# Kernel optimization log

Hardware: AMD Instinct MI355X
Metric: run time of the kernel (lower is better)

## Reference

```python
import jax, jax.numpy as jnp
import numpy as np

B, T, N, F = 4, 24, 1024, 96
H, HD = 3, 32      # spatial GATConv: 3 heads, head-dim 32 (averaged -> 32 per branch, 3 branches -> 96)
GH, GHD = 4, 24    # GroupedGAT: 4 heads concatenated -> 96
E = 8192           # edges per graph


def setup_inputs() -> dict:
    key = jax.random.key(0)
    ks = jax.random.split(key, 24)
    s_in = 1.0 / np.sqrt(F)
    def gat_params(k):
        k1, k2, k3, k4 = jax.random.split(k, 4)
        return (jax.random.normal(k1, (F, H * HD), jnp.float32) * s_in,
                jax.random.normal(k2, (H, HD), jnp.float32) * 0.1,
                jax.random.normal(k3, (H, HD), jnp.float32) * 0.1,
                jax.random.normal(k4, (H, HD), jnp.float32) * 0.02)
    W_d, al_d, ar_d, b_d = gat_params(ks[3])
    W_m, al_m, ar_m, b_m = gat_params(ks[4])
    W_s, al_s, ar_s, b_s = gat_params(ks[5])
    inp = {
        "input": jax.random.normal(ks[0], (B, T, N, F), jnp.float32),
        "spatial_embedding": jax.random.normal(ks[1], (B, T, N, F), jnp.float32),
        "temporal_embedding": jax.random.normal(ks[2], (B, T, N, F), jnp.float32),
        "src_d": jax.random.randint(ks[6], (E,), 0, N, jnp.int32),
        "dst_d": (jnp.arange(E) % N).astype(jnp.int32),
        "src_m": jax.random.randint(ks[7], (E,), 0, N, jnp.int32),
        "dst_m": (jnp.arange(E) % N).astype(jnp.int32),
        "src_s": jax.random.randint(ks[8], (E,), 0, N, jnp.int32),
        "dst_s": (jnp.arange(E) % N).astype(jnp.int32),
        "W_d": W_d, "al_d": al_d, "ar_d": ar_d, "b_d": b_d,
        "W_m": W_m, "al_m": al_m, "ar_m": ar_m, "b_m": b_m,
        "W_s": W_s, "al_s": al_s, "ar_s": ar_s, "b_s": b_s,
        "Wg": jax.random.normal(ks[9], (F, GH * GHD), jnp.float32) * s_in,
        "agl": jax.random.normal(ks[10], (GH, GHD), jnp.float32) * 0.1,
        "agr": jax.random.normal(ks[11], (GH, GHD), jnp.float32) * 0.1,
        "Wf": jax.random.normal(ks[12], (2 * F, F), jnp.float32) * (1.0 / np.sqrt(2 * F)),
        "bf": jnp.zeros((F,), jnp.float32),
    }
    return inp


def _gat(x, src, dst, W, al, ar, b):
    # x: (N, K, F) node features with K = T*B batched feature slots
    K = x.shape[1]
    h = (x @ W).reshape(N, K, H, HD)                       # (N,K,H,HD)
    el = (h * al).sum(-1)                                  # (N,K,H)
    er = (h * ar).sum(-1)
    e = jax.nn.leaky_relu(el[src] + er[dst], 0.2)          # (E,K,H)
    emax = jax.ops.segment_max(e, dst, num_segments=N)
    emax = jnp.where(jnp.isfinite(emax), emax, 0.0)
    ex = jnp.exp(e - emax[dst])
    denom = jax.ops.segment_sum(ex, dst, num_segments=N)
    alpha = ex / (denom[dst] + 1e-9)                       # edge softmax over incoming edges
    out = jax.ops.segment_sum(h[src] * alpha[..., None], dst, num_segments=N)
    return (out + b).mean(2)                               # average heads -> (N,K,HD)


def reference(input, spatial_embedding, temporal_embedding,
              src_d, dst_d, src_m, dst_m, src_s, dst_s,
              W_d, al_d, ar_d, b_d, W_m, al_m, ar_m, b_m, W_s, al_s, ar_s, b_s,
              Wg, agl, agr, Wf, bf):
    # ---------------- SpatialBlock ----------------
    residual_s = input                                     # input_dim == output_dim
    x_in = input + spatial_embedding
    # torch: input.transpose(0,2).reshape(N,-1,F) -> slot order is (t,b)
    x = jnp.transpose(x_in, (2, 1, 0, 3)).reshape(N, T * B, F)
    xd = _gat(x, src_d, dst_d, W_d, al_d, ar_d, b_d)
    xm = _gat(x, src_m, dst_m, W_m, al_m, ar_m, b_m)
    xs = _gat(x, src_s, dst_s, W_s, al_s, ar_s, b_s)
    x_attn = jnp.concatenate([xd, xm, xs], axis=-1)        # (N, T*B, 3*HD=F)
    # torch: transpose(0,1).reshape(batch,T,N,-1)  (keeps original (t,b) slot order quirk)
    x_attn = jnp.transpose(x_attn, (1, 0, 2)).reshape(B, T, N, F)
    cov0 = spatial_embedding[:, 0]                         # (B,N,F)
    attn_S = jax.nn.softmax(cov0 @ jnp.swapaxes(cov0, 1, 2), axis=2)  # (B,N,N)
    # NOTE: embedding_x branch in SpatialBlock is dead code (out is overwritten); skipped.
    spatial = residual_s + x_attn

    # ---------------- TemporalBlock ----------------
    residual_t = input
    xt = jnp.swapaxes(input, 1, 2).reshape(B * N, T, F)    # (B*N, T, F), index k=b*N+n
    # GroupedGAT: dense multi-head GAT over the T=period_num time steps
    hg = (xt @ Wg).reshape(B * N, T, GH, GHD)
    elg = (hg * agl).sum(-1)                               # (BN,T,GH)
    erg = (hg * agr).sum(-1)
    eg = jax.nn.leaky_relu(elg[:, :, None, :] + erg[:, None, :, :], 0.2)  # (BN,Ti,Tj,GH)
    alphag = jax.nn.softmax(eg, axis=2)
    xg = jnp.einsum('kijh,kjhd->kihd', alphag, hg).reshape(B * N, T, GH * GHD)
    covT = temporal_embedding[:, :, 0]                     # (B,T,F)
    attn_T = jax.nn.softmax(covT @ jnp.swapaxes(covT, 1, 2), axis=1)      # softmax over dim=1 as in torch
    # torch: attn.repeat(N,1,1) paired with x of batch index b*N+n -> uses attn[(b*N+n) % B]
    idx = (jnp.arange(B * N) % B)
    emb = jnp.einsum('kij,kjf->kif', attn_T[idx], xt)      # (BN,T,F)
    xg = xg * jax.nn.sigmoid(emb)
    xg = jnp.swapaxes(xg.reshape(B, N, T, F), 1, 2)        # (B,T,N,F)
    temporal = residual_t + xg

    # ---------------- Fusion ----------------
    z = jax.nn.sigmoid(jnp.concatenate([spatial, temporal], axis=-1) @ Wf + bf)
    out = z * spatial + (1.0 - z) * temporal + input
    return out, attn_S
```

## Files before the change

kernel.cpp:

```cpp
#include <hip/hip_runtime.h>
#include <hip/hip_bf16.h>

typedef long long i64;
typedef __attribute__((ext_vector_type(8))) short short8b;
typedef __attribute__((ext_vector_type(4))) short short4b;
typedef __attribute__((ext_vector_type(4))) float f32x4;

union U8 { short8b v; ushort s[8]; };
union U4 { short4b v; ushort s[4]; };

static __device__ __forceinline__ float bs2f(ushort u) {
    union { unsigned int i; float f; } x; x.i = ((unsigned int)u) << 16; return x.f;
}
static __device__ __forceinline__ ushort f2bs(float f) {
    __hip_bfloat16 h = __float2bfloat16(f);
    return *reinterpret_cast<ushort*>(&h);
}
static __device__ __forceinline__ void mfma_bf16(f32x4& acc, short8b a, short8b b) {
    asm volatile("v_mfma_f32_16x16x32_bf16 %0, %1, %2, %0" : "+v"(acc) : "v"(a), "v"(b));
}
static __device__ __forceinline__ void mfma_fence() {
    asm volatile("s_nop 7\n\ts_nop 7\n\ts_nop 7");
}


__global__ __launch_bounds__(256) void prep_weights_kernel(
        const float* __restrict__ Wd, const float* __restrict__ Wm,
        const float* __restrict__ Ws, const float* __restrict__ Wg,
        const float* __restrict__ Wf,
        const float* __restrict__ ald, const float* __restrict__ ard,
        const float* __restrict__ alm, const float* __restrict__ arm,
        const float* __restrict__ als, const float* __restrict__ ars,
        const float* __restrict__ agl, const float* __restrict__ agr,
        ushort* __restrict__ wtab) {
    int idx = blockIdx.x * 256 + threadIdx.x;
    if (idx >= 61440) return;
    if (idx < 43008) {
        int w = idx / 10752, rem = idx - w * 10752;
        int c = rem / 96, k = rem - c * 96;
        float v;
        if (w < 3) {
            const float* W = (w == 0) ? Wd : (w == 1) ? Wm : Ws;
            if (c < 96) {
                v = W[k * 96 + c];
            } else {
                int j = c - 96, h = j >> 1;
                const float* a = (j & 1) ? ((w == 0) ? ard : (w == 1) ? arm : ars)
                                         : ((w == 0) ? ald : (w == 1) ? alm : als);
                v = 0.f;
                for (int d = 0; d < 32; ++d) v += W[k * 96 + h * 32 + d] * a[h * 32 + d];
            }
        } else {
            if (c < 96) {
                v = Wg[k * 96 + c];
            } else {
                int j = c - 96, g = j & 3;
                const float* a = (j >> 2) ? agr : agl;
                v = 0.f;
                for (int d = 0; d < 24; ++d) v += Wg[k * 96 + g * 24 + d] * a[g * 24 + d];
            }
        }
        wtab[w * 10752 + c * 96 + k] = f2bs(v);
    } else {
        int rem = idx - 43008;
        int c = rem / 192, k = rem - c * 192;
        wtab[43008 + c * 192 + k] = f2bs(Wf[k * 96 + c]);
    }
}

__global__ __launch_bounds__(256) void build_x_kernel(const float* __restrict__ inp,
                                                      const float* __restrict__ spat,
                                                      ushort* __restrict__ x) {
    int i4 = blockIdx.x * 256 + threadIdx.x;
    int q = i4 % 24;
    int r = i4 / 24;
    int n = r & 1023, bt = r >> 10;
    int t = bt % 24, b = bt / 24;
    int k = t * 4 + b;
    float4 a = ((const float4*)inp)[i4];
    float4 s = ((const float4*)spat)[i4];
    U4 u;
    u.s[0] = f2bs(a.x + s.x); u.s[1] = f2bs(a.y + s.y);
    u.s[2] = f2bs(a.z + s.z); u.s[3] = f2bs(a.w + s.w);
    *(short4b*)&x[((i64)((k << 10) | n)) * 96 + q * 4] = u.v;
}

__global__ __launch_bounds__(256) void gemm96_mfma_kernel(const ushort* __restrict__ X,
                                                          const ushort* __restrict__ wt,
                                                          ushort* __restrict__ Ho,
                                                          float* __restrict__ el,
                                                          float* __restrict__ er) {
    __shared__ ushort Xs[128 * 104];
    __shared__ ushort Wt[112 * 104];
    int tid = threadIdx.x;
    i64 row0 = (i64)blockIdx.x * 128;
    for (int i = tid; i < 1344; i += 256) {
        int c = i / 12, kg = i - c * 12;
        *(short8b*)&Wt[c * 104 + kg * 8] = *(const short8b*)&wt[c * 96 + kg * 8];
    }
    for (int i = tid; i < 1536; i += 256) {
        int r = i / 12, q = i - r * 12;
        *(short8b*)&Xs[r * 104 + q * 8] = *(const short8b*)&X[(row0 + r) * 96 + q * 8];
    }
    __syncthreads();
    int wid = tid >> 6, lane = tid & 63;
    int lr = lane & 15, lk = lane >> 4;
    f32x4 acc[2][7];
#pragma unroll
    for (int m = 0; m < 2; ++m)
#pragma unroll
        for (int c = 0; c < 7; ++c) acc[m][c] = (f32x4){0.f, 0.f, 0.f, 0.f};
    const ushort* xa = &Xs[(wid * 32 + lr) * 104 + lk * 8];
    const ushort* wb = &Wt[lr * 104 + lk * 8];
#pragma unroll
    for (int ks = 0; ks < 3; ++ks) {
        short8b a0 = *(const short8b*)(xa + ks * 32);
        short8b a1 = *(const short8b*)(xa + 16 * 104 + ks * 32);
#pragma unroll
        for (int c = 0; c < 7; ++c) {
            short8b b = *(const short8b*)(wb + c * 16 * 104 + ks * 32);
            mfma_bf16(acc[0][c], a0, b);
            mfma_bf16(acc[1][c], a1, b);
        }
    }
    mfma_fence();
#pragma unroll
    for (int m = 0; m < 2; ++m) {
#pragma unroll
        for (int c = 0; c < 6; ++c)
#pragma unroll
            for (int r = 0; r < 4; ++r) {
                i64 row = row0 + wid * 32 + m * 16 + lk * 4 + r;
                Ho[row * 96 + c * 16 + lr] = f2bs(acc[m][c][r]);
            }
        if (lr < 6) {
            float* dst = (lr & 1) ? er : el;
            int h = lr >> 1;
#pragma unroll
            for (int r = 0; r < 4; ++r) {
                i64 row = row0 + wid * 32 + m * 16 + lk * 4 + r;
                dst[row * 3 + h] = acc[m][6][r];
            }
        }
    }
}

__global__ __launch_bounds__(256) void gemm96_hg_mfma_kernel(const float* __restrict__ inp,
                                                             const ushort* __restrict__ wt,
                                                             ushort* __restrict__ Ho,
                                                             float* __restrict__ elg,
                                                             float* __restrict__ erg) {
    __shared__ ushort Xs[128 * 104];
    __shared__ ushort Wt[112 * 104];
    int tid = threadIdx.x;
    i64 row0 = (i64)blockIdx.x * 128;
    for (int i = tid; i < 1344; i += 256) {
        int c = i / 12, kg = i - c * 12;
        *(short8b*)&Wt[c * 104 + kg * 8] = *(const short8b*)&wt[c * 96 + kg * 8];
    }
    for (int i = tid; i < 3072; i += 256) {
        int r = i / 24, q = i - r * 24;
        int row = (int)row0 + r;
        int kk = row / 24, t = row - kk * 24;
        int b = kk >> 10, n = kk & 1023;
        float4 v = ((const float4*)inp)[((i64)(((b * 24 + t) << 10) | n)) * 24 + q];
        U4 u;
        u.s[0] = f2bs(v.x); u.s[1] = f2bs(v.y); u.s[2] = f2bs(v.z); u.s[3] = f2bs(v.w);
        *(short4b*)&Xs[r * 104 + q * 4] = u.v;
    }
    __syncthreads();
    int wid = tid >> 6, lane = tid & 63;
    int lr = lane & 15, lk = lane >> 4;
    f32x4 acc[2][7];
#pragma unroll
    for (int m = 0; m < 2; ++m)
#pragma unroll
        for (int c = 0; c < 7; ++c) acc[m][c] = (f32x4){0.f, 0.f, 0.f, 0.f};
    const ushort* xa = &Xs[(wid * 32 + lr) * 104 + lk * 8];
    const ushort* wb = &Wt[lr * 104 + lk * 8];
#pragma unroll
    for (int ks = 0; ks < 3; ++ks) {
        short8b a0 = *(const short8b*)(xa + ks * 32);
        short8b a1 = *(const short8b*)(xa + 16 * 104 + ks * 32);
#pragma unroll
        for (int c = 0; c < 7; ++c) {
            short8b b = *(const short8b*)(wb + c * 16 * 104 + ks * 32);
            mfma_bf16(acc[0][c], a0, b);
            mfma_bf16(acc[1][c], a1, b);
        }
    }
    mfma_fence();
#pragma unroll
    for (int m = 0; m < 2; ++m) {
#pragma unroll
        for (int c = 0; c < 6; ++c)
#pragma unroll
            for (int r = 0; r < 4; ++r) {
                i64 row = row0 + wid * 32 + m * 16 + lk * 4 + r;
                Ho[row * 96 + c * 16 + lr] = f2bs(acc[m][c][r]);
            }
        if (lr < 8) {
            float* dst = (lr >> 2) ? erg : elg;
            int g = lr & 3;
#pragma unroll
            for (int r = 0; r < 4; ++r) {
                i64 row = row0 + wid * 32 + m * 16 + lk * 4 + r;
                dst[row * 4 + g] = acc[m][6][r];
            }
        }
    }
}

__global__ __launch_bounds__(256) void gat_agg_kernel(const ushort* __restrict__ H2,
                                                      const float* __restrict__ el,
                                                      const float* __restrict__ er,
                                                      const int* __restrict__ src,
                                                      const float* __restrict__ bv,
                                                      ushort* __restrict__ xattn,
                                                      int g) {
    int tid = threadIdx.x;
    int pp = tid >> 3, l8 = tid & 7;
    int p = blockIdx.x * 32 + pp;
    int k = p >> 10, n = p & 1023;
    int d0 = l8 * 4;
    int s[8];
#pragma unroll
    for (int j = 0; j < 8; ++j) s[j] = src[n + j * 1024];
    float acc[4] = {0.f, 0.f, 0.f, 0.f};
#pragma unroll
    for (int h = 0; h < 3; ++h) {
        float erv = er[((i64)((k << 10) | n)) * 3 + h];
        float e[8];
        float m = -1e30f;
#pragma unroll
        for (int j = 0; j < 8; ++j) {
            float ev = el[((i64)((k << 10) | s[j])) * 3 + h] + erv;
            ev = ev >= 0.f ? ev : 0.2f * ev;
            e[j] = ev;
            m = fmaxf(m, ev);
        }
        float sum = 0.f;
#pragma unroll
        for (int j = 0; j < 8; ++j) { e[j] = expf(e[j] - m); sum += e[j]; }
        float inv = 1.f / (sum + 1e-9f);
        float o[4] = {0.f, 0.f, 0.f, 0.f};
#pragma unroll
        for (int j = 0; j < 8; ++j) {
            U4 hv; hv.v = *(const short4b*)&H2[((i64)((k << 10) | s[j])) * 96 + h * 32 + d0];
#pragma unroll
            for (int c = 0; c < 4; ++c) o[c] += e[j] * bs2f(hv.s[c]);
        }
#pragma unroll
        for (int c = 0; c < 4; ++c) acc[c] += o[c] * inv + bv[h * 32 + d0 + c];
    }
    U4 u;
#pragma unroll
    for (int c = 0; c < 4; ++c) u.s[c] = f2bs(acc[c] * (1.f / 3.f));
    *(short4b*)&xattn[((i64)((k << 10) | n)) * 96 + g * 32 + d0] = u.v;
}

__global__ __launch_bounds__(256) void attn_scores_kernel(const float* __restrict__ spat,
                                                          float* __restrict__ attnS) {
    int bid = blockIdx.x;
    int b = bid >> 8;
    int i0 = ((bid >> 4) & 15) * 64;
    int j0 = (bid & 15) * 64;
    const float* C = spat + (i64)b * 24 * 1024 * 96;
    __shared__ __align__(16) float As[64 * 100];
    __shared__ __align__(16) float Bs[64 * 100];
    int tid = threadIdx.x;
    float4* As4 = (float4*)As;
    float4* Bs4 = (float4*)Bs;
    const float4* Ai = (const float4*)(C + (i64)i0 * 96);
    const float4* Bj = (const float4*)(C + (i64)j0 * 96);
    for (int i = tid; i < 1536; i += 256) {
        int row = i / 24, q = i - row * 24;
        As4[row * 25 + q] = Ai[i];
        Bs4[row * 25 + q] = Bj[i];
    }
    __syncthreads();
    int tj = tid & 15, ti = tid >> 4;
    float acc[4][4];
#pragma unroll
    for (int r = 0; r < 4; ++r)
#pragma unroll
        for (int s = 0; s < 4; ++s) acc[r][s] = 0.f;
    for (int k4 = 0; k4 < 24; ++k4) {
        float4 a[4], bv[4];
#pragma unroll
        for (int r = 0; r < 4; ++r) a[r] = As4[(ti * 4 + r) * 25 + k4];
#pragma unroll
        for (int s = 0; s < 4; ++s) bv[s] = Bs4[(s * 16 + tj) * 25 + k4];
#pragma unroll
        for (int r = 0; r < 4; ++r)
#pragma unroll
            for (int s = 0; s < 4; ++s)
                acc[r][s] += a[r].x * bv[s].x + a[r].y * bv[s].y + a[r].z * bv[s].z + a[r].w * bv[s].w;
    }
#pragma unroll
    for (int r = 0; r < 4; ++r) {
        i64 orow = ((i64)(b << 10) + i0 + ti * 4 + r) * 1024 + j0;
#pragma unroll
        for (int s = 0; s < 4; ++s) attnS[orow + s * 16 + tj] = acc[r][s];
    }
}

__global__ __launch_bounds__(256) void attn_softmax_kernel(float* __restrict__ attnS) {
    i64 base = (i64)blockIdx.x * 1024;
    float4* row4 = (float4*)(attnS + base);
    int tid = threadIdx.x;
    float4 v = row4[tid];
    __shared__ float red[256];
    float m = fmaxf(fmaxf(v.x, v.y), fmaxf(v.z, v.w));
    red[tid] = m;
    __syncthreads();
    for (int st = 128; st > 0; st >>= 1) {
        if (tid < st) red[tid] = fmaxf(red[tid], red[tid + st]);
        __syncthreads();
    }
    m = red[0];
    __syncthreads();
    v.x = expf(v.x - m); v.y = expf(v.y - m); v.z = expf(v.z - m); v.w = expf(v.w - m);
    red[tid] = v.x + v.y + v.z + v.w;
    __syncthreads();
    for (int st = 128; st > 0; st >>= 1) {
        if (tid < st) red[tid] += red[tid + st];
        __syncthreads();
    }
    float inv = 1.f / red[0];
    v.x *= inv; v.y *= inv; v.z *= inv; v.w *= inv;
    row4[tid] = v;
}

__global__ __launch_bounds__(576) void attn_t_kernel(const float* __restrict__ temp,
                                                     float* __restrict__ attnT) {
    int b = blockIdx.x;
    int tid = threadIdx.x;
    __shared__ float cs[24][96];
    __shared__ float M[24][24];
    for (int i = tid; i < 2304; i += 576) {
        int r = i / 96, f = i - r * 96;
        cs[r][f] = temp[((i64)(b * 24 + r)) * 1024 * 96 + f];
    }
    __syncthreads();
    int i = tid / 24, j = tid - i * 24;
    float s = 0.f;
#pragma unroll
    for (int f = 0; f < 96; ++f) s += cs[i][f] * cs[j][f];
    M[i][j] = s;
    __syncthreads();
    float m = -1e30f;
#pragma unroll
    for (int i2 = 0; i2 < 24; ++i2) m = fmaxf(m, M[i2][j]);
    float sum = 0.f;
#pragma unroll
    for (int i2 = 0; i2 < 24; ++i2) sum += expf(M[i2][j] - m);
    attnT[((i64)b * 24 + i) * 24 + j] = expf(M[i][j] - m) / sum;
}

__global__ __launch_bounds__(192) void temporal_kernel(const float* __restrict__ inp,
                                                       const ushort* __restrict__ hg,
                                                       const float* __restrict__ elgb,
                                                       const float* __restrict__ ergb,
                                                       const float* __restrict__ attnT,
                                                       ushort* __restrict__ gated) {
    int kk = blockIdx.x;
    int b = kk >> 10, n = kk & 1023;
    __shared__ __align__(16) float hgs[24 * 100];
    __shared__ __align__(16) float xs[24 * 100];
    __shared__ float at[24 * 24];
    __shared__ __align__(16) float elg[24][4];
    __shared__ __align__(16) float erg[24][4];
    __shared__ float alpha[4][24][24];
    int tid = threadIdx.x;
    for (int i = tid; i < 576; i += 192) {
        int r = i / 24, q = i - r * 24;
        U4 u; u.v = *(const short4b*)&hg[(i64)kk * 2304 + r * 96 + q * 4];
        float4 v;
        v.x = bs2f(u.s[0]); v.y = bs2f(u.s[1]); v.z = bs2f(u.s[2]); v.w = bs2f(u.s[3]);
        *(float4*)&hgs[r * 100 + q * 4] = v;
    }
    for (int i = tid; i < 576; i += 192) {
        int r = i / 24, q = i - r * 24;
        *(float4*)&xs[r * 100 + q * 4] =
            ((const float4*)inp)[(((i64)(b * 24 + r)) << 10 | n) * 24 + q];
    }
    int ib = kk & 3;
    for (int i = tid; i < 576; i += 192) at[i] = attnT[ib * 576 + i];
    for (int i = tid; i < 48; i += 192) {
        int r = i >> 1;
        if (i & 1) *(float4*)&erg[r][0] = ((const float4*)ergb)[(i64)kk * 24 + r];
        else       *(float4*)&elg[r][0] = ((const float4*)elgb)[(i64)kk * 24 + r];
    }
    __syncthreads();
    if (tid < 96) {
        int i = tid >> 2, g = tid & 3;
        float ev[24];
        float m = -1e30f;
        float eli = elg[i][g];
#pragma unroll
        for (int j = 0; j < 24; ++j) {
            float e = eli + erg[j][g];
            e = e >= 0.f ? e : 0.2f * e;
            ev[j] = e;
            m = fmaxf(m, e);
        }
        float sum = 0.f;
#pragma unroll
        for (int j = 0; j < 24; ++j) { ev[j] = expf(ev[j] - m); sum += ev[j]; }
        float inv = 1.f / sum;
#pragma unroll
        for (int j = 0; j < 24; ++j) alpha[g][i][j] = ev[j] * inv;
    }
    __syncthreads();
#pragma unroll
    for (int s2 = 0; s2 < 3; ++s2) {
        int idx = tid + s2 * 192;
        int i = idx / 24, f4 = idx - i * 24;
        int g = f4 / 6;
        const float* ap = &alpha[g][i][0];
        const float* atp = &at[i * 24];
        float4 xg = {0.f, 0.f, 0.f, 0.f}, emb = {0.f, 0.f, 0.f, 0.f};
#pragma unroll 8
        for (int j = 0; j < 24; ++j) {
            float a = ap[j], w = atp[j];
            float4 h4 = *(const float4*)&hgs[j * 100 + f4 * 4];
            float4 x4 = *(const float4*)&xs[j * 100 + f4 * 4];
            xg.x += a * h4.x; xg.y += a * h4.y; xg.z += a * h4.z; xg.w += a * h4.w;
            emb.x += w * x4.x; emb.y += w * x4.y; emb.z += w * x4.z; emb.w += w * x4.w;
        }
        U4 o;
        o.s[0] = f2bs(xg.x / (1.f + expf(-emb.x)));
        o.s[1] = f2bs(xg.y / (1.f + expf(-emb.y)));
        o.s[2] = f2bs(xg.z / (1.f + expf(-emb.z)));
        o.s[3] = f2bs(xg.w / (1.f + expf(-emb.w)));
        *(short4b*)&gated[(i64)kk * 2304 + i * 96 + f4 * 4] = o.v;
    }
}

__global__ __launch_bounds__(256) void fusion_mfma_kernel(const float* __restrict__ inp,
                                                          const ushort* __restrict__ xattn,
                                                          const ushort* __restrict__ gated,
                                                          const ushort* __restrict__ wtf,
                                                          const float* __restrict__ bfv,
                                                          float* __restrict__ outb) {
    __shared__ ushort Xs[64 * 200];
    __shared__ ushort Wt[96 * 200];
    int tid = threadIdx.x;
    i64 row0 = (i64)blockIdx.x * 64;
    for (int i = tid; i < 2304; i += 256) {
        int c = i / 24, kg = i - c * 24;
        *(short8b*)&Wt[c * 200 + kg * 8] = *(const short8b*)&wtf[c * 192 + kg * 8];
    }
    for (int i = tid; i < 768; i += 256) {
        int r = i / 12, q = i - r * 12;
        i64 grow = row0 + r;
        int n = (int)(grow & 1023);
        int bt = (int)(grow >> 10);
        int t = bt % 24, b = bt / 24;
        float4 iv0 = ((const float4*)inp)[grow * 24 + q * 2];
        float4 iv1 = ((const float4*)inp)[grow * 24 + q * 2 + 1];
        U8 xa; xa.v = *(const short8b*)&xattn[grow * 96 + q * 8];
        U8 gd; gd.v = *(const short8b*)&gated[(((i64)((b << 10) | n)) * 24 + t) * 96 + q * 8];
        float ivf[8] = {iv0.x, iv0.y, iv0.z, iv0.w, iv1.x, iv1.y, iv1.z, iv1.w};
        U8 sp, tm;
#pragma unroll
        for (int j = 0; j < 8; ++j) {
            sp.s[j] = f2bs(ivf[j] + bs2f(xa.s[j]));
            tm.s[j] = f2bs(ivf[j] + bs2f(gd.s[j]));
        }
        *(short8b*)&Xs[r * 200 + q * 8] = sp.v;
        *(short8b*)&Xs[r * 200 + 96 + q * 8] = tm.v;
    }
    __syncthreads();
    int wid = tid >> 6, lane = tid & 63;
    int lr = lane & 15, lk = lane >> 4;
    f32x4 acc[6];
#pragma unroll
    for (int c = 0; c < 6; ++c) acc[c] = (f32x4){0.f, 0.f, 0.f, 0.f};
    const ushort* xa = &Xs[(wid * 16 + lr) * 200 + lk * 8];
    const ushort* wb = &Wt[lr * 200 + lk * 8];
#pragma unroll
    for (int ks = 0; ks < 6; ++ks) {
        short8b a = *(const short8b*)(xa + ks * 32);
#pragma unroll
        for (int c = 0; c < 6; ++c) {
            short8b b = *(const short8b*)(wb + c * 16 * 200 + ks * 32);
            mfma_bf16(acc[c], a, b);
        }
    }
    mfma_fence();
#pragma unroll
    for (int c = 0; c < 6; ++c) {
        int col = c * 16 + lr;
        float bfc = bfv[col];
#pragma unroll
        for (int r = 0; r < 4; ++r) {
            int lrow = wid * 16 + lk * 4 + r;
            i64 grow = row0 + lrow;
            float z = 1.f / (1.f + expf(-(acc[c][r] + bfc)));
            float sp = bs2f(Xs[lrow * 200 + col]);
            float tm = bs2f(Xs[lrow * 200 + 96 + col]);
            float iv = inp[grow * 96 + col];
            outb[grow * 96 + col] = z * sp + (1.f - z) * tm + iv;
        }
    }
}

extern "C" void kernel_launch(void* const* d_in, const int* in_sizes, int n_in,
                              void* d_out, int out_size, void* d_ws, size_t ws_size,
                              hipStream_t stream) {
    const float* input = (const float*)d_in[0];
    const float* spat  = (const float*)d_in[1];
    const float* temp  = (const float*)d_in[2];
    const int* src_d = (const int*)d_in[3];
    const int* src_m = (const int*)d_in[5];
    const int* src_s = (const int*)d_in[7];
    const float* W_d  = (const float*)d_in[9];
    const float* al_d = (const float*)d_in[10];
    const float* ar_d = (const float*)d_in[11];
    const float* b_d  = (const float*)d_in[12];
    const float* W_m  = (const float*)d_in[13];
    const float* al_m = (const float*)d_in[14];
    const float* ar_m = (const float*)d_in[15];
    const float* b_m  = (const float*)d_in[16];
    const float* W_s  = (const float*)d_in[17];
    const float* al_s = (const float*)d_in[18];
    const float* ar_s = (const float*)d_in[19];
    const float* b_s  = (const float*)d_in[20];
    const float* Wg   = (const float*)d_in[21];
    const float* agl  = (const float*)d_in[22];
    const float* agr  = (const float*)d_in[23];
    const float* Wf   = (const float*)d_in[24];
    const float* bf_  = (const float*)d_in[25];

    float* outb  = (float*)d_out;
    float* attnS = outb + 9437184;

    float* wsf = (float*)d_ws;
    ushort* xbf      = (ushort*)wsf;
    ushort* hgbf     = xbf;
    ushort* H2bf     = (ushort*)(wsf + 4718592);
    ushort* gatedbf  = H2bf;
    ushort* xattnbf  = (ushort*)(wsf + 9437184);
    float* el    = wsf + 14155776;
    float* er    = el + 294912;
    float* elgb  = wsf + 14155776;
    float* attnT = wsf + 14745600;
    float* ergb  = wsf + 14747904;
    ushort* wtab = (ushort*)(wsf + 15141120);
    ushort* wt_d = wtab;
    ushort* wt_m = wtab + 10752;
    ushort* wt_s = wtab + 21504;
    ushort* wtg  = wtab + 32256;
    ushort* wtf  = wtab + 43008;

    prep_weights_kernel<<<240, 256, 0, stream>>>(W_d, W_m, W_s, Wg, Wf,
                                                 al_d, ar_d, al_m, ar_m, al_s, ar_s,
                                                 agl, agr, wtab);
    build_x_kernel<<<9216, 256, 0, stream>>>(input, spat, xbf);

    const ushort* Wgat[3] = {wt_d, wt_m, wt_s};
    const float* bgat[3] = {b_d, b_m, b_s};
    const int* srcs[3] = {src_d, src_m, src_s};
    for (int g = 0; g < 3; ++g) {
        gemm96_mfma_kernel<<<768, 256, 0, stream>>>(xbf, Wgat[g], H2bf, el, er);
        gat_agg_kernel<<<3072, 256, 0, stream>>>(H2bf, el, er, srcs[g], bgat[g],
                                                 xattnbf, g);
    }

    attn_scores_kernel<<<1024, 256, 0, stream>>>(spat, attnS);
    attn_softmax_kernel<<<4096, 256, 0, stream>>>(attnS);

    gemm96_hg_mfma_kernel<<<768, 256, 0, stream>>>(input, wtg, hgbf, elgb, ergb);
    attn_t_kernel<<<4, 576, 0, stream>>>(temp, attnT);
    temporal_kernel<<<4096, 192, 0, stream>>>(input, hgbf, elgb, ergb, attnT, gatedbf);
    fusion_mfma_kernel<<<1536, 256, 0, stream>>>(input, xattnbf, gatedbf, wtf, bf_, outb);
}
```

Measured before the change: 272.1 us.

## Distribute GAT edge softmax via shuffles and register-tile temporal kernel over rows

In the GAT aggregation kernel, each of the 8 lanes per node now loads one edge's source index and logits, and the per-head max and sum come from 8-lane shuffle reductions instead of every lane repeating all 8 edges. The per-edge weights are broadcast by shuffle, and the bias is summed once at the end. In the temporal kernel, hg and x are kept as bf16 in shared memory, and x is rounded from fp32 to bf16, which adds precision loss. Alpha and the temporal attention are stored transposed so each thread computes 3 output rows per column group, reusing each shared-memory load across rows, and all 192 threads now take part in the softmax.

```diff
diff --git a/kernel.cpp b/kernel.cpp
--- a/kernel.cpp
+++ b/kernel.cpp
@@ -223,40 +223,58 @@
     int p = blockIdx.x * 32 + pp;
     int k = p >> 10, n = p & 1023;
     int d0 = l8 * 4;
-    int s[8];
-#pragma unroll
-    for (int j = 0; j < 8; ++j) s[j] = src[n + j * 1024];
+    i64 kb = (i64)(k << 10);
+    int s_own = src[n + l8 * 1024];
+    const float* elp = &el[(kb | s_own) * 3];
+    const float* erp = &er[(kb | n) * 3];
+    float e[3], m[3];
+#pragma unroll
+    for (int h = 0; h < 3; ++h) {
+        float ev = elp[h] + erp[h];
+        e[h] = ev >= 0.f ? ev : 0.2f * ev;
+        m[h] = e[h];
+    }
+#pragma unroll
+    for (int mask = 1; mask < 8; mask <<= 1) {
+#pragma unroll
+        for (int h = 0; h < 3; ++h) m[h] = fmaxf(m[h], __shfl_xor(m[h], mask, 8));
+    }
+    float pex[3], S[3];
+#pragma unroll
+    for (int h = 0; h < 3; ++h) { pex[h] = expf(e[h] - m[h]); S[h] = pex[h]; }
+#pragma unroll
+    for (int mask = 1; mask < 8; mask <<= 1) {
+#pragma unroll
+        for (int h = 0; h < 3; ++h) S[h] += __shfl_xor(S[h], mask, 8);
+    }
+    float w[3];
+#pragma unroll
+    for (int h = 0; h < 3; ++h) w[h] = pex[h] / (S[h] + 1e-9f);
     float acc[4] = {0.f, 0.f, 0.f, 0.f};
 #pragma unroll
-    for (int h = 0; h < 3; ++h) {
-        float erv = er[((i64)((k << 10) | n)) * 3 + h];
-        float e[8];
-        float m = -1e30f;
-#pragma unroll
-        for (int j = 0; j < 8; ++j) {
-            float ev = el[((i64)((k << 10) | s[j])) * 3 + h] + erv;
-            ev = ev >= 0.f ? ev : 0.2f * ev;
-            e[j] = ev;
-            m = fmaxf(m, ev);
-        }
-        float sum = 0.f;
-#pragma unroll
-        for (int j = 0; j < 8; ++j) { e[j] = expf(e[j] - m); sum += e[j]; }
-        float inv = 1.f / (sum + 1e-9f);
-        float o[4] = {0.f, 0.f, 0.f, 0.f};
-#pragma unroll
-        for (int j = 0; j < 8; ++j) {
-            U4 hv; hv.v = *(const short4b*)&H2[((i64)((k << 10) | s[j])) * 96 + h * 32 + d0];
-#pragma unroll
-            for (int c = 0; c < 4; ++c) o[c] += e[j] * bs2f(hv.s[c]);
-        }
-#pragma unroll
-        for (int c = 0; c < 4; ++c) acc[c] += o[c] * inv + bv[h * 32 + d0 + c];
-    }
+    for (int j = 0; j < 8; ++j) {
+        int sj = __shfl(s_own, j, 8);
+        float a0 = __shfl(w[0], j, 8);
+        float a1 = __shfl(w[1], j, 8);
+        float a2 = __shfl(w[2], j, 8);
+        const ushort* hp = &H2[(kb | sj) * 96 + d0];
+        U4 h0, h1, h2;
+        h0.v = *(const short4b*)&hp[0];
+        h1.v = *(const short4b*)&hp[32];
+        h2.v = *(const short4b*)&hp[64];
+#pragma unroll
+        for (int c = 0; c < 4; ++c)
+            acc[c] += a0 * bs2f(h0.s[c]) + a1 * bs2f(h1.s[c]) + a2 * bs2f(h2.s[c]);
+    }
+    float4 b0 = *(const float4*)&bv[d0];
+    float4 b1 = *(const float4*)&bv[32 + d0];
+    float4 b2 = *(const float4*)&bv[64 + d0];
+    float bsum[4] = {b0.x + b1.x + b2.x, b0.y + b1.y + b2.y,
+                     b0.z + b1.z + b2.z, b0.w + b1.w + b2.w};
     U4 u;
 #pragma unroll
-    for (int c = 0; c < 4; ++c) u.s[c] = f2bs(acc[c] * (1.f / 3.f));
-    *(short4b*)&xattn[((i64)((k << 10) | n)) * 96 + g * 32 + d0] = u.v;
+    for (int c = 0; c < 4; ++c) u.s[c] = f2bs((acc[c] + bsum[c]) * (1.f / 3.f));
+    *(short4b*)&xattn[(kb | n) * 96 + g * 32 + d0] = u.v;
 }
 
 __global__ __launch_bounds__(256) void attn_scores_kernel(const float* __restrict__ spat,
@@ -366,75 +384,87 @@
                                                        ushort* __restrict__ gated) {
     int kk = blockIdx.x;
     int b = kk >> 10, n = kk & 1023;
-    __shared__ __align__(16) float hgs[24 * 100];
-    __shared__ __align__(16) float xs[24 * 100];
-    __shared__ float at[24 * 24];
-    __shared__ __align__(16) float elg[24][4];
-    __shared__ __align__(16) float erg[24][4];
-    __shared__ float alpha[4][24][24];
-    int tid = threadIdx.x;
+    __shared__ __align__(16) ushort hgs[24 * 96];
+    __shared__ __align__(16) ushort xs[24 * 96];
+    __shared__ __align__(16) float alphaT[4][24][32];
+    __shared__ __align__(16) float atT[24][32];
+    __shared__ __align__(16) float elg[24][4], erg[24][4];
+    int tid = threadIdx.x;
+    for (int i = tid; i < 576; i += 192)
+        *(short4b*)&hgs[i * 4] = *(const short4b*)&hg[(i64)kk * 2304 + i * 4];
     for (int i = tid; i < 576; i += 192) {
         int r = i / 24, q = i - r * 24;
-        U4 u; u.v = *(const short4b*)&hg[(i64)kk * 2304 + r * 96 + q * 4];
-        float4 v;
-        v.x = bs2f(u.s[0]); v.y = bs2f(u.s[1]); v.z = bs2f(u.s[2]); v.w = bs2f(u.s[3]);
-        *(float4*)&hgs[r * 100 + q * 4] = v;
-    }
+        float4 v = ((const float4*)inp)[(((i64)(b * 24 + r)) << 10 | n) * 24 + q];
+        U4 u;
+        u.s[0] = f2bs(v.x); u.s[1] = f2bs(v.y); u.s[2] = f2bs(v.z); u.s[3] = f2bs(v.w);
+        *(short4b*)&xs[r * 96 + q * 4] = u.v;
+    }
+    int ib = kk & 3;
     for (int i = tid; i < 576; i += 192) {
-        int r = i / 24, q = i - r * 24;
-        *(float4*)&xs[r * 100 + q * 4] =
-            ((const float4*)inp)[(((i64)(b * 24 + r)) << 10 | n) * 24 + q];
-    }
-    int ib = kk & 3;
-    for (int i = tid; i < 576; i += 192) at[i] = attnT[ib * 576 + i];
+        int ii = i / 24, j = i - ii * 24;
+        atT[j][(ii / 3) * 4 + (ii - (ii / 3) * 3)] = attnT[ib * 576 + i];
+    }
     for (int i = tid; i < 48; i += 192) {
         int r = i >> 1;
         if (i & 1) *(float4*)&erg[r][0] = ((const float4*)ergb)[(i64)kk * 24 + r];
         else       *(float4*)&elg[r][0] = ((const float4*)elgb)[(i64)kk * 24 + r];
     }
     __syncthreads();
-    if (tid < 96) {
-        int i = tid >> 2, g = tid & 3;
-        float ev[24];
+    {
+        int i = tid >> 3, g = (tid >> 1) & 3, half = tid & 1;
+        int j0 = half * 12;
+        float eli = elg[i][g];
+        float ev[12];
         float m = -1e30f;
-        float eli = elg[i][g];
-#pragma unroll
-        for (int j = 0; j < 24; ++j) {
-            float e = eli + erg[j][g];
+#pragma unroll
+        for (int j = 0; j < 12; ++j) {
+            float e = eli + erg[j0 + j][g];
             e = e >= 0.f ? e : 0.2f * e;
             ev[j] = e;
             m = fmaxf(m, e);
         }
+        m = fmaxf(m, __shfl_xor(m, 1));
         float sum = 0.f;
 #pragma unroll
-        for (int j = 0; j < 24; ++j) { ev[j] = expf(ev[j] - m); sum += ev[j]; }
+        for (int j = 0; j < 12; ++j) { ev[j] = expf(ev[j] - m); sum += ev[j]; }
+        sum += __shfl_xor(sum, 1);
         float inv = 1.f / sum;
-#pragma unroll
-        for (int j = 0; j < 24; ++j) alpha[g][i][j] = ev[j] * inv;
-    }
-    __syncthreads();
-#pragma unroll
-    for (int s2 = 0; s2 < 3; ++s2) {
-        int idx = tid + s2 * 192;
-        int i = idx / 24, f4 = idx - i * 24;
-        int g = f4 / 6;
-        const float* ap = &alpha[g][i][0];
-        const float* atp = &at[i * 24];
-        float4 xg = {0.f, 0.f, 0.f, 0.f}, emb = {0.f, 0.f, 0.f, 0.f};
-#pragma unroll 8
-        for (int j = 0; j < 24; ++j) {
-            float a = ap[j], w = atp[j];
-            float4 h4 = *(const float4*)&hgs[j * 100 + f4 * 4];
-            float4 x4 = *(const float4*)&xs[j * 100 + f4 * 4];
-            xg.x += a * h4.x; xg.y += a * h4.y; xg.z += a * h4.z; xg.w += a * h4.w;
-            emb.x += w * x4.x; emb.y += w * x4.y; emb.z += w * x4.z; emb.w += w * x4.w;
-        }
+        int slot = (i / 3) * 4 + (i - (i / 3) * 3);
+#pragma unroll
+        for (int j = 0; j < 12; ++j) alphaT[g][j0 + j][slot] = ev[j] * inv;
+    }
+    __syncthreads();
+    int ig = tid / 24, f4 = tid - (tid / 24) * 24;
+    int g = f4 / 6;
+    float4 xg0 = {0,0,0,0}, xg1 = {0,0,0,0}, xg2 = {0,0,0,0};
+    float4 em0 = {0,0,0,0}, em1 = {0,0,0,0}, em2 = {0,0,0,0};
+#pragma unroll
+    for (int j = 0; j < 24; ++j) {
+        U4 uh, ux;
+        uh.v = *(const short4b*)&hgs[j * 96 + f4 * 4];
+        ux.v = *(const short4b*)&xs[j * 96 + f4 * 4];
+        float4 a4 = *(const float4*)&alphaT[g][j][ig * 4];
+        float4 w4 = *(const float4*)&atT[j][ig * 4];
+        float h0 = bs2f(uh.s[0]), h1 = bs2f(uh.s[1]), h2 = bs2f(uh.s[2]), h3 = bs2f(uh.s[3]);
+        float x0 = bs2f(ux.s[0]), x1 = bs2f(ux.s[1]), x2 = bs2f(ux.s[2]), x3 = bs2f(ux.s[3]);
+        xg0.x += a4.x * h0; xg0.y += a4.x * h1; xg0.z += a4.x * h2; xg0.w += a4.x * h3;
+        xg1.x += a4.y * h0; xg1.y += a4.y * h1; xg1.z += a4.y * h2; xg1.w += a4.y * h3;
+        xg2.x += a4.z * h0; xg2.y += a4.z * h1; xg2.z += a4.z * h2; xg2.w += a4.z * h3;
+        em0.x += w4.x * x0; em0.y += w4.x * x1; em0.z += w4.x * x2; em0.w += w4.x * x3;
+        em1.x += w4.y * x0; em1.y += w4.y * x1; em1.z += w4.y * x2; em1.w += w4.y * x3;
+        em2.x += w4.z * x0; em2.y += w4.z * x1; em2.z += w4.z * x2; em2.w += w4.z * x3;
+    }
+    i64 obase = (i64)kk * 2304 + f4 * 4;
+#pragma unroll
+    for (int r = 0; r < 3; ++r) {
+        float4 xg = (r == 0) ? xg0 : (r == 1) ? xg1 : xg2;
+        float4 em = (r == 0) ? em0 : (r == 1) ? em1 : em2;
         U4 o;
-        o.s[0] = f2bs(xg.x / (1.f + expf(-emb.x)));
-        o.s[1] = f2bs(xg.y / (1.f + expf(-emb.y)));
-        o.s[2] = f2bs(xg.z / (1.f + expf(-emb.z)));
-        o.s[3] = f2bs(xg.w / (1.f + expf(-emb.w)));
-        *(short4b*)&gated[(i64)kk * 2304 + i * 96 + f4 * 4] = o.v;
+        o.s[0] = f2bs(xg.x / (1.f + expf(-em.x)));
+        o.s[1] = f2bs(xg.y / (1.f + expf(-em.y)));
+        o.s[2] = f2bs(xg.z / (1.f + expf(-em.z)));
+        o.s[3] = f2bs(xg.w / (1.f + expf(-em.w)));
+        *(short4b*)&gated[obase + (i64)(ig * 3 + r) * 96] = o.v;
     }
 }
 
```

Measured after the change: 245.1 us. -9.9%, faster.
